# Optimization experiments

Measured on AMD Instinct MI355X. Metric: run time of the kernel, lower is better.

## Reference

```python
import jax, jax.numpy as jnp
import numpy as np

D_MODEL = 2048
N_HEAD = 16
HEAD_DIM = D_MODEL // N_HEAD
SCALE = 1.0 / (HEAD_DIM ** 0.5)


def setup_inputs() -> dict:
    key = jax.random.key(0)
    kx, kq, kk, kv, ko = jax.random.split(key, 5)
    std = 1.0 / np.sqrt(D_MODEL)
    return {
        "x": jax.random.normal(kx, (2, 2048, D_MODEL), dtype=jnp.float32),
        "w_q": jax.random.normal(kq, (D_MODEL, D_MODEL), dtype=jnp.float32) * std,
        "w_k": jax.random.normal(kk, (D_MODEL, D_MODEL), dtype=jnp.float32) * std,
        "w_v": jax.random.normal(kv, (D_MODEL, D_MODEL), dtype=jnp.float32) * std,
        "w_o": jax.random.normal(ko, (D_MODEL, D_MODEL), dtype=jnp.float32) * std,
    }


def reference(x, w_q, w_k, w_v, w_o):
    b, s, d = x.shape
    # nn.Linear(d,d,bias=False): y = x @ W^T, weights stored [out, in]
    def proj(w):
        y = jnp.einsum("bsd,ed->bse", x, w)
        return y.reshape(b, s, N_HEAD, HEAD_DIM).transpose(0, 2, 1, 3)  # [b,h,s,hd]
    q, k, v = proj(w_q), proj(w_k), proj(w_v)
    scores = jnp.einsum("bhqd,bhkd->bhqk", q, k) * SCALE  # [b,h,s,s]
    probs = jax.nn.softmax(scores, axis=-1)
    attn = jnp.einsum("bhqk,bhkd->bhqd", probs, v)
    attn = attn.transpose(0, 2, 1, 3).reshape(b, s, d)
    return jnp.einsum("bsd,ed->bse", attn, w_o)
```

## Files before the change

### kernel.cpp

```cpp
#include <hip/hip_runtime.h>

#define D_MODEL 2048
#define SEQ 2048
#define BATCH 2
#define NH 16
#define HD 128
#define MTOT 4096
#define NQKV 6144
#define QSTRIDE 4096

static constexpr float SCALE_LOG2E = 0.08838834764831845f * 1.4426950408889634f;

typedef __bf16 bf16x8 __attribute__((ext_vector_type(8)));
typedef _Float16 f16x4 __attribute__((ext_vector_type(4)));
typedef float f32x4 __attribute__((ext_vector_type(4)));

__device__ inline unsigned short f2bf(float f) {
  unsigned int u = __builtin_bit_cast(unsigned int, f);
  u += 0x7fffu + ((u >> 16) & 1u);
  return (unsigned short)(u >> 16);
}

__device__ inline float fast_exp2(float x) {
#if __has_builtin(__builtin_amdgcn_exp2f)
  return __builtin_amdgcn_exp2f(x);
#else
  return exp2f(x);
#endif
}

__device__ inline void gload_lds16(const void* g, void* s) {
  __builtin_amdgcn_global_load_lds(
      (__attribute__((address_space(1))) void*)g,
      (__attribute__((address_space(3))) void*)s, 16, 0, 0);
}

__global__ __launch_bounds__(256) void cvt_all(
    const float* __restrict__ x, const float* __restrict__ wq,
    const float* __restrict__ wk, const float* __restrict__ wv,
    const float* __restrict__ wo, unsigned short* __restrict__ xb,
    unsigned short* __restrict__ wqkv, unsigned short* __restrict__ wob) {
  const int y = blockIdx.y;
  const float* src;
  unsigned short* dst;
  int n4;
  if (y == 0) { src = x; dst = xb; n4 = MTOT * D_MODEL / 4; }
  else if (y == 4) { src = wo; dst = wob; n4 = D_MODEL * D_MODEL / 4; }
  else {
    src = (y == 1) ? wq : (y == 2) ? wk : wv;
    dst = wqkv + (size_t)(y - 1) * D_MODEL * D_MODEL;
    n4 = D_MODEL * D_MODEL / 4;
  }
  int i = blockIdx.x * 256 + threadIdx.x;
  if (i < n4) {
    float4 v = ((const float4*)src)[i];
    ushort4 o;
    o.x = f2bf(v.x); o.y = f2bf(v.y); o.z = f2bf(v.z); o.w = f2bf(v.w);
    ((ushort4*)dst)[i] = o;
  }
}

__global__ __launch_bounds__(256, 2) void gemm_qkv(
    const unsigned short* __restrict__ A, const unsigned short* __restrict__ B,
    unsigned short* __restrict__ QK, unsigned short* __restrict__ Vt) {
  __shared__ __align__(16) union {
    struct { unsigned short As[128 * 32]; unsigned short Bs[128 * 32]; } s;
    unsigned short T[128 * 136];
  } u;
  unsigned short* As = u.s.As;
  unsigned short* Bs = u.s.Bs;
  const int K = D_MODEL;
  const int tid = threadIdx.x;
  const int lane = tid & 63;
  const int wave = tid >> 6;
  const int quad = lane >> 4;
  const int l15 = lane & 15;
  const int m0 = blockIdx.y * 128;
  const int n0 = blockIdx.x * 128;
  const int wm = (wave >> 1) * 64;
  const int wn = (wave & 1) * 64;

  const int c0 = wave * 2, c1 = wave * 2 + 1;
  const int srow = lane >> 2;
  const int sr0 = c0 * 16 + srow;
  const int sr1 = c1 * 16 + srow;
  const int sk = (((lane & 3) ^ (srow & 3))) * 8;
  const unsigned short* Ag0 = A + (size_t)(m0 + sr0) * K + sk;
  const unsigned short* Ag1 = A + (size_t)(m0 + sr1) * K + sk;
  const unsigned short* Bg0 = B + (size_t)(n0 + sr0) * K + sk;
  const unsigned short* Bg1 = B + (size_t)(n0 + sr1) * K + sk;
  unsigned short* lA0 = As + c0 * 512;
  unsigned short* lA1 = As + c1 * 512;
  unsigned short* lB0 = Bs + c0 * 512;
  unsigned short* lB1 = Bs + c1 * 512;

  f32x4 acc[4][4] = {};
  const int axor = (quad ^ (l15 & 3)) * 8;

  for (int k0 = 0; k0 < K; k0 += 32) {
    __syncthreads();
    gload_lds16(Ag0 + k0, lA0);
    gload_lds16(Ag1 + k0, lA1);
    gload_lds16(Bg0 + k0, lB0);
    gload_lds16(Bg1 + k0, lB1);
    __builtin_amdgcn_s_waitcnt(0);
    __syncthreads();
    bf16x8 a[4], b[4];
#pragma unroll
    for (int i = 0; i < 4; i++)
      a[i] = *(const bf16x8*)(As + (wm + i * 16 + l15) * 32 + axor);
#pragma unroll
    for (int j = 0; j < 4; j++)
      b[j] = *(const bf16x8*)(Bs + (wn + j * 16 + l15) * 32 + axor);
#pragma unroll
    for (int i = 0; i < 4; i++)
#pragma unroll
      for (int j = 0; j < 4; j++)
        acc[i][j] = __builtin_amdgcn_mfma_f32_16x16x32_bf16(a[i], b[j], acc[i][j], 0, 0, 0);
  }

  const int er = quad * 4;
  const int ec = l15;
  if (n0 < 4096) {
#pragma unroll
    for (int i = 0; i < 4; i++)
#pragma unroll
      for (int j = 0; j < 4; j++) {
        const int mm = m0 + wm + i * 16 + er;
        const int nn = n0 + wn + j * 16 + ec;
#pragma unroll
        for (int r = 0; r < 4; r++)
          QK[(size_t)(mm + r) * QSTRIDE + nn] = f2bf(acc[i][j][r]);
      }
  } else {
    __syncthreads();
    const int vcol0 = n0 - 4096;
    const int h = vcol0 >> 7;
    const int b = m0 >> 11;
    const int bh = b * NH + h;
    const int sbase = m0 & (SEQ - 1);
#pragma unroll
    for (int i = 0; i < 4; i++)
#pragma unroll
      for (int j = 0; j < 4; j++) {
        const int dl = wn + j * 16 + ec;
        const int sl = wm + i * 16 + er;
        f16x4 hv;
#pragma unroll
        for (int r = 0; r < 4; r++) hv[r] = (_Float16)acc[i][j][r];
        *(f16x4*)(u.T + dl * 136 + sl) = hv;
      }
    __syncthreads();
#pragma unroll
    for (int p = 0; p < 8; p++) {
      const int d = p * 16 + (tid >> 4);
      const int s = (tid & 15) * 8;
      float4 chunk = *(const float4*)(u.T + d * 136 + s);
      *(float4*)(Vt + ((size_t)(bh * HD + d)) * SEQ + sbase + s) = chunk;
    }
  }
}

__global__ __launch_bounds__(256, 4) void gemm_out(
    const unsigned short* __restrict__ A, const unsigned short* __restrict__ B,
    float* __restrict__ C, int M, int N, int K) {
  __shared__ __align__(16) unsigned short As[128 * 32];
  __shared__ __align__(16) unsigned short Bs[64 * 32];
  const int tid = threadIdx.x;
  const int lane = tid & 63;
  const int wave = tid >> 6;
  const int quad = lane >> 4;
  const int l15 = lane & 15;
  const int m0 = blockIdx.y * 128;
  const int n0 = blockIdx.x * 64;
  const int wm = (wave >> 1) * 64;
  const int wn = (wave & 1) * 32;

  const int srow = lane >> 2;
  const int sk = (((lane & 3) ^ (srow & 3))) * 8;
  const unsigned short* Ag0 = A + (size_t)(m0 + wave * 32 + srow) * K + sk;
  const unsigned short* Ag1 = A + (size_t)(m0 + wave * 32 + 16 + srow) * K + sk;
  unsigned short* lA0 = As + (wave * 2) * 512;
  unsigned short* lA1 = As + (wave * 2 + 1) * 512;
  const unsigned short* Bg = B + (size_t)(n0 + wave * 16 + srow) * K + sk;
  unsigned short* lB = Bs + wave * 512;

  f32x4 acc[4][2] = {};
  const int axor = (quad ^ (l15 & 3)) * 8;

  for (int k0 = 0; k0 < K; k0 += 32) {
    __syncthreads();
    gload_lds16(Ag0 + k0, lA0);
    gload_lds16(Ag1 + k0, lA1);
    gload_lds16(Bg + k0, lB);
    __builtin_amdgcn_s_waitcnt(0);
    __syncthreads();
    bf16x8 a[4], b[2];
#pragma unroll
    for (int i = 0; i < 4; i++)
      a[i] = *(const bf16x8*)(As + (wm + i * 16 + l15) * 32 + axor);
#pragma unroll
    for (int j = 0; j < 2; j++)
      b[j] = *(const bf16x8*)(Bs + (wn + j * 16 + l15) * 32 + axor);
#pragma unroll
    for (int i = 0; i < 4; i++)
#pragma unroll
      for (int j = 0; j < 2; j++)
        acc[i][j] = __builtin_amdgcn_mfma_f32_16x16x32_bf16(a[i], b[j], acc[i][j], 0, 0, 0);
  }

  const int er = quad * 4;
  const int ec = l15;
#pragma unroll
  for (int i = 0; i < 4; i++)
#pragma unroll
    for (int j = 0; j < 2; j++) {
      const int mm = m0 + wm + i * 16 + er;
      const int nn = n0 + wn + j * 16 + ec;
#pragma unroll
      for (int r = 0; r < 4; r++)
        C[(size_t)(mm + r) * N + nn] = acc[i][j][r];
    }
}

__global__ __launch_bounds__(256, 2) void flash_attn(
    const unsigned short* __restrict__ QK, const unsigned short* __restrict__ Vt,
    unsigned short* __restrict__ Og) {
  __shared__ __align__(16) unsigned short Ks[2][64 * 128];
  __shared__ __align__(16) unsigned short Vs[2][128 * 64];
  const int tid = threadIdx.x;
  const int lane = tid & 63;
  const int wave = tid >> 6;
  const int quad = lane >> 4;
  const int l15 = lane & 15;
  const int id = blockIdx.x;
  const int xr = id & 7;
  const int kk = id >> 3;
  const int bh = xr * 4 + (kk >> 4);
  const int b = bh >> 4, h = bh & 15;
  const int q0 = (kk & 15) * 128;

  const size_t kbase = (size_t)(b * SEQ) * QSTRIDE + D_MODEL + h * HD;
  const size_t vbase = (size_t)bh * HD * SEQ;

  bf16x8 qf[2][4];
#pragma unroll
  for (int t = 0; t < 2; t++)
#pragma unroll
    for (int kc = 0; kc < 4; kc++)
      qf[t][kc] = *(const bf16x8*)(QK + (size_t)(b * SEQ + q0 + wave * 32 + t * 16 + l15) * QSTRIDE +
                                   h * HD + kc * 32 + quad * 8);

  const unsigned short* kg[4];
  const unsigned short* vg[4];
  int klofs[4], vlofs[4];
#pragma unroll
  for (int i = 0; i < 4; i++) {
    int krow = wave * 16 + i * 4 + quad;
    int kc_ = l15 ^ (i * 4 + quad);
    kg[i] = QK + kbase + (size_t)krow * QSTRIDE + kc_ * 8;
    klofs[i] = (wave * 16 + i * 4) * 128;
    int vrow = wave * 32 + i * 8 + (lane >> 3);
    int vc_ = (lane & 7) ^ (lane >> 3);
    vg[i] = Vt + vbase + (size_t)vrow * SEQ + vc_ * 8;
    vlofs[i] = (wave * 32 + i * 8) * 64;
  }

#pragma unroll
  for (int i = 0; i < 4; i++) gload_lds16(kg[i], &Ks[0][klofs[i]]);
#pragma unroll
  for (int i = 0; i < 4; i++) gload_lds16(vg[i], &Vs[0][vlofs[i]]);
#pragma unroll
  for (int i = 0; i < 4; i++) { kg[i] += 64 * QSTRIDE; vg[i] += 64; }
  __builtin_amdgcn_s_waitcnt(0);
  __syncthreads();

  float lsum[2] = {0.f, 0.f};
  f32x4 Oa[2][8] = {};

  for (int it = 0; it < SEQ / 64; ++it) {
    const int cur = it & 1;
    if (it < SEQ / 64 - 1) {
#pragma unroll
      for (int i = 0; i < 4; i++) gload_lds16(kg[i], &Ks[cur ^ 1][klofs[i]]);
#pragma unroll
      for (int i = 0; i < 4; i++) gload_lds16(vg[i], &Vs[cur ^ 1][vlofs[i]]);
#pragma unroll
      for (int i = 0; i < 4; i++) { kg[i] += 64 * QSTRIDE; vg[i] += 64; }
    }

    const unsigned short* kb = &Ks[cur][0];
    f32x4 sacc[2][4] = {};
#pragma unroll
    for (int js = 0; js < 4; js++)
#pragma unroll
      for (int kc = 0; kc < 4; kc++) {
        bf16x8 kf = *(const bf16x8*)(kb + (js * 16 + l15) * 128 + (((kc * 4 + quad) ^ l15) * 8));
        sacc[0][js] = __builtin_amdgcn_mfma_f32_16x16x32_bf16(kf, qf[0][kc], sacc[0][js], 0, 0, 0);
        sacc[1][js] = __builtin_amdgcn_mfma_f32_16x16x32_bf16(kf, qf[1][kc], sacc[1][js], 0, 0, 0);
      }

    f16x4 pb[2][4];
#pragma unroll
    for (int t = 0; t < 2; t++)
#pragma unroll
      for (int js = 0; js < 4; js++)
#pragma unroll
        for (int r = 0; r < 4; r++) {
          float p = fast_exp2(sacc[t][js][r] * SCALE_LOG2E);
          lsum[t] += p;
          pb[t][js][r] = (_Float16)p;
        }

    const unsigned short* vb_ = &Vs[cur][0];
#pragma unroll
    for (int jt = 0; jt < 8; jt++)
#pragma unroll
      for (int js = 0; js < 4; js++) {
        f16x4 vf = *(const f16x4*)(vb_ + (jt * 16 + l15) * 64 +
                                   (((js * 2 + (quad >> 1)) ^ (lane & 7)) * 8) + (quad & 1) * 4);
        Oa[0][jt] = __builtin_amdgcn_mfma_f32_16x16x16f16(vf, pb[0][js], Oa[0][jt], 0, 0, 0);
        Oa[1][jt] = __builtin_amdgcn_mfma_f32_16x16x16f16(vf, pb[1][js], Oa[1][jt], 0, 0, 0);
      }

    __builtin_amdgcn_s_waitcnt(0);
    __syncthreads();
  }

  float inv[2];
#pragma unroll
  for (int t = 0; t < 2; t++) {
    float s = lsum[t];
    s += __shfl_xor(s, 16);
    s += __shfl_xor(s, 32);
    inv[t] = 1.0f / s;
  }

#pragma unroll
  for (int t = 0; t < 2; t++) {
    const size_t rowbase = (size_t)(b * SEQ + q0 + wave * 32 + t * 16 + l15) * D_MODEL + h * HD;
#pragma unroll
    for (int jt = 0; jt < 8; jt++) {
      ushort4 o;
      o.x = f2bf(Oa[t][jt][0] * inv[t]);
      o.y = f2bf(Oa[t][jt][1] * inv[t]);
      o.z = f2bf(Oa[t][jt][2] * inv[t]);
      o.w = f2bf(Oa[t][jt][3] * inv[t]);
      *(ushort4*)(Og + rowbase + jt * 16 + quad * 4) = o;
    }
  }
}

extern "C" void kernel_launch(void* const* d_in, const int* in_sizes, int n_in,
                              void* d_out, int out_size, void* d_ws, size_t ws_size,
                              hipStream_t stream) {
  const float* x = (const float*)d_in[0];
  const float* wq = (const float*)d_in[1];
  const float* wk = (const float*)d_in[2];
  const float* wv = (const float*)d_in[3];
  const float* wo = (const float*)d_in[4];
  float* out = (float*)d_out;
  char* ws = (char*)d_ws;
  const size_t MB = 1u << 20;
  if (ws_size < 96 * MB) return;

  unsigned short* xb = (unsigned short*)(ws);
  unsigned short* wqkv = (unsigned short*)(ws + 16 * MB);
  unsigned short* wob = (unsigned short*)(ws + 40 * MB);
  unsigned short* QKb = (unsigned short*)(ws + 48 * MB);
  unsigned short* Vtb = (unsigned short*)(ws + 80 * MB);
  unsigned short* Ab = xb;

  cvt_all<<<dim3(8192, 5), 256, 0, stream>>>(x, wq, wk, wv, wo, xb, wqkv, wob);

  gemm_qkv<<<dim3(NQKV / 128, MTOT / 128), 256, 0, stream>>>(xb, wqkv, QKb, Vtb);

  flash_attn<<<512, 256, 0, stream>>>(QKb, Vtb, Ab);

  gemm_out<<<dim3(D_MODEL / 64, MTOT / 128), 256, 0, stream>>>(Ab, wob, out, MTOT, D_MODEL, D_MODEL);
}
```

Measured before the change: 392.4 us.

## Split Q/K buffers, widen attention blocks to 8 waves, split-K output GEMM

The fused QK buffer becomes separate contiguous Q and K buffers, so K rows load with stride D_MODEL instead of 4096. Flash attention now runs 512 threads per block, with each wave owning 16 query rows instead of 32. This halves per-wave registers and shares each K/V tile across more waves, though it doubles the LDS reads per MFMA. The output GEMM moves to 128x128 tiles with two wave groups, each handling half of K, and the partial sums are reduced through LDS. That raises arithmetic intensity but adds a serialized reduction epilogue and fewer blocks.

```diff
diff --git a/kernel.cpp b/kernel.cpp
--- a/kernel.cpp
+++ b/kernel.cpp
@@ -7,7 +7,6 @@
 #define HD 128
 #define MTOT 4096
 #define NQKV 6144
-#define QSTRIDE 4096
 
 static constexpr float SCALE_LOG2E = 0.08838834764831845f * 1.4426950408889634f;
 
@@ -62,7 +61,8 @@
 
 __global__ __launch_bounds__(256, 2) void gemm_qkv(
     const unsigned short* __restrict__ A, const unsigned short* __restrict__ B,
-    unsigned short* __restrict__ QK, unsigned short* __restrict__ Vt) {
+    unsigned short* __restrict__ Qb, unsigned short* __restrict__ Kb,
+    unsigned short* __restrict__ Vt) {
   __shared__ __align__(16) union {
     struct { unsigned short As[128 * 32]; unsigned short Bs[128 * 32]; } s;
     unsigned short T[128 * 136];
@@ -82,13 +82,11 @@
 
   const int c0 = wave * 2, c1 = wave * 2 + 1;
   const int srow = lane >> 2;
-  const int sr0 = c0 * 16 + srow;
-  const int sr1 = c1 * 16 + srow;
   const int sk = (((lane & 3) ^ (srow & 3))) * 8;
-  const unsigned short* Ag0 = A + (size_t)(m0 + sr0) * K + sk;
-  const unsigned short* Ag1 = A + (size_t)(m0 + sr1) * K + sk;
-  const unsigned short* Bg0 = B + (size_t)(n0 + sr0) * K + sk;
-  const unsigned short* Bg1 = B + (size_t)(n0 + sr1) * K + sk;
+  const unsigned short* Ag0 = A + (size_t)(m0 + c0 * 16 + srow) * K + sk;
+  const unsigned short* Ag1 = A + (size_t)(m0 + c1 * 16 + srow) * K + sk;
+  const unsigned short* Bg0 = B + (size_t)(n0 + c0 * 16 + srow) * K + sk;
+  const unsigned short* Bg1 = B + (size_t)(n0 + c1 * 16 + srow) * K + sk;
   unsigned short* lA0 = As + c0 * 512;
   unsigned short* lA1 = As + c1 * 512;
   unsigned short* lB0 = Bs + c0 * 512;
@@ -122,15 +120,17 @@
   const int er = quad * 4;
   const int ec = l15;
   if (n0 < 4096) {
+    unsigned short* Dst = (n0 < 2048) ? Qb : Kb;
+    const int nb = (n0 < 2048) ? n0 : (n0 - 2048);
 #pragma unroll
     for (int i = 0; i < 4; i++)
 #pragma unroll
       for (int j = 0; j < 4; j++) {
         const int mm = m0 + wm + i * 16 + er;
-        const int nn = n0 + wn + j * 16 + ec;
+        const int nn = nb + wn + j * 16 + ec;
 #pragma unroll
         for (int r = 0; r < 4; r++)
-          QK[(size_t)(mm + r) * QSTRIDE + nn] = f2bf(acc[i][j][r]);
+          Dst[(size_t)(mm + r) * D_MODEL + nn] = f2bf(acc[i][j][r]);
       }
   } else {
     __syncthreads();
@@ -161,71 +161,89 @@
   }
 }
 
-__global__ __launch_bounds__(256, 4) void gemm_out(
+__global__ __launch_bounds__(512, 4) void gemm_out(
     const unsigned short* __restrict__ A, const unsigned short* __restrict__ B,
     float* __restrict__ C, int M, int N, int K) {
-  __shared__ __align__(16) unsigned short As[128 * 32];
-  __shared__ __align__(16) unsigned short Bs[64 * 32];
+  __shared__ __align__(16) unsigned short As[2][128 * 32];
+  __shared__ __align__(16) unsigned short Bs[2][128 * 32];
   const int tid = threadIdx.x;
   const int lane = tid & 63;
   const int wave = tid >> 6;
+  const int g = wave >> 2;
+  const int w = wave & 3;
   const int quad = lane >> 4;
   const int l15 = lane & 15;
   const int m0 = blockIdx.y * 128;
-  const int n0 = blockIdx.x * 64;
-  const int wm = (wave >> 1) * 64;
-  const int wn = (wave & 1) * 32;
-
+  const int n0 = blockIdx.x * 128;
+  const int wm = (w >> 1) * 64;
+  const int wn = (w & 1) * 64;
+  const int kb = g * (D_MODEL / 2);
+
+  const int c0 = w * 2, c1 = w * 2 + 1;
   const int srow = lane >> 2;
   const int sk = (((lane & 3) ^ (srow & 3))) * 8;
-  const unsigned short* Ag0 = A + (size_t)(m0 + wave * 32 + srow) * K + sk;
-  const unsigned short* Ag1 = A + (size_t)(m0 + wave * 32 + 16 + srow) * K + sk;
-  unsigned short* lA0 = As + (wave * 2) * 512;
-  unsigned short* lA1 = As + (wave * 2 + 1) * 512;
-  const unsigned short* Bg = B + (size_t)(n0 + wave * 16 + srow) * K + sk;
-  unsigned short* lB = Bs + wave * 512;
-
-  f32x4 acc[4][2] = {};
+  const unsigned short* Ag0 = A + (size_t)(m0 + c0 * 16 + srow) * K + kb + sk;
+  const unsigned short* Ag1 = A + (size_t)(m0 + c1 * 16 + srow) * K + kb + sk;
+  const unsigned short* Bg0 = B + (size_t)(n0 + c0 * 16 + srow) * K + kb + sk;
+  const unsigned short* Bg1 = B + (size_t)(n0 + c1 * 16 + srow) * K + kb + sk;
+  unsigned short* lA0 = As[g] + c0 * 512;
+  unsigned short* lA1 = As[g] + c1 * 512;
+  unsigned short* lB0 = Bs[g] + c0 * 512;
+  unsigned short* lB1 = Bs[g] + c1 * 512;
+
+  f32x4 acc[4][4] = {};
   const int axor = (quad ^ (l15 & 3)) * 8;
 
-  for (int k0 = 0; k0 < K; k0 += 32) {
+  for (int k0 = 0; k0 < D_MODEL / 2; k0 += 32) {
     __syncthreads();
     gload_lds16(Ag0 + k0, lA0);
     gload_lds16(Ag1 + k0, lA1);
-    gload_lds16(Bg + k0, lB);
+    gload_lds16(Bg0 + k0, lB0);
+    gload_lds16(Bg1 + k0, lB1);
     __builtin_amdgcn_s_waitcnt(0);
     __syncthreads();
-    bf16x8 a[4], b[2];
-#pragma unroll
-    for (int i = 0; i < 4; i++)
-      a[i] = *(const bf16x8*)(As + (wm + i * 16 + l15) * 32 + axor);
-#pragma unroll
-    for (int j = 0; j < 2; j++)
-      b[j] = *(const bf16x8*)(Bs + (wn + j * 16 + l15) * 32 + axor);
-#pragma unroll
-    for (int i = 0; i < 4; i++)
-#pragma unroll
-      for (int j = 0; j < 2; j++)
+    bf16x8 a[4], b[4];
+#pragma unroll
+    for (int i = 0; i < 4; i++)
+      a[i] = *(const bf16x8*)(As[g] + (wm + i * 16 + l15) * 32 + axor);
+#pragma unroll
+    for (int j = 0; j < 4; j++)
+      b[j] = *(const bf16x8*)(Bs[g] + (wn + j * 16 + l15) * 32 + axor);
+#pragma unroll
+    for (int i = 0; i < 4; i++)
+#pragma unroll
+      for (int j = 0; j < 4; j++)
         acc[i][j] = __builtin_amdgcn_mfma_f32_16x16x32_bf16(a[i], b[j], acc[i][j], 0, 0, 0);
   }
 
-  const int er = quad * 4;
-  const int ec = l15;
-#pragma unroll
-  for (int i = 0; i < 4; i++)
-#pragma unroll
-    for (int j = 0; j < 2; j++) {
-      const int mm = m0 + wm + i * 16 + er;
-      const int nn = n0 + wn + j * 16 + ec;
-#pragma unroll
-      for (int r = 0; r < 4; r++)
-        C[(size_t)(mm + r) * N + nn] = acc[i][j][r];
+  float* R = (float*)&As[0][0];
+  const int ridx = w * 1104 + lane * 17;
+#pragma unroll 1
+  for (int i = 0; i < 4; i++) {
+    __syncthreads();
+    if (g == 1) {
+#pragma unroll
+      for (int j = 0; j < 4; j++)
+#pragma unroll
+        for (int r = 0; r < 4; r++) R[ridx + j * 4 + r] = acc[i][j][r];
     }
-}
-
-__global__ __launch_bounds__(256, 2) void flash_attn(
-    const unsigned short* __restrict__ QK, const unsigned short* __restrict__ Vt,
-    unsigned short* __restrict__ Og) {
+    __syncthreads();
+    if (g == 0) {
+      const int mm = m0 + wm + i * 16 + quad * 4;
+#pragma unroll
+      for (int j = 0; j < 4; j++) {
+        const int nn = n0 + wn + j * 16 + l15;
+#pragma unroll
+        for (int r = 0; r < 4; r++)
+          C[(size_t)(mm + r) * N + nn] = acc[i][j][r] + R[ridx + j * 4 + r];
+      }
+    }
+  }
+}
+
+__global__ __launch_bounds__(512, 4) void flash_attn(
+    const unsigned short* __restrict__ Q, const unsigned short* __restrict__ Kg,
+    const unsigned short* __restrict__ Vt, unsigned short* __restrict__ Og) {
   __shared__ __align__(16) unsigned short Ks[2][64 * 128];
   __shared__ __align__(16) unsigned short Vs[2][128 * 64];
   const int tid = threadIdx.x;
@@ -234,83 +252,77 @@
   const int quad = lane >> 4;
   const int l15 = lane & 15;
   const int id = blockIdx.x;
-  const int xr = id & 7;
-  const int kk = id >> 3;
-  const int bh = xr * 4 + (kk >> 4);
+  const int bh = id >> 4;
   const int b = bh >> 4, h = bh & 15;
-  const int q0 = (kk & 15) * 128;
-
-  const size_t kbase = (size_t)(b * SEQ) * QSTRIDE + D_MODEL + h * HD;
+  const int q0 = (id & 15) * 128;
+
+  const size_t kbase = (size_t)(b * SEQ) * D_MODEL + h * HD;
   const size_t vbase = (size_t)bh * HD * SEQ;
 
-  bf16x8 qf[2][4];
-#pragma unroll
-  for (int t = 0; t < 2; t++)
-#pragma unroll
-    for (int kc = 0; kc < 4; kc++)
-      qf[t][kc] = *(const bf16x8*)(QK + (size_t)(b * SEQ + q0 + wave * 32 + t * 16 + l15) * QSTRIDE +
-                                   h * HD + kc * 32 + quad * 8);
-
-  const unsigned short* kg[4];
-  const unsigned short* vg[4];
-  int klofs[4], vlofs[4];
-#pragma unroll
-  for (int i = 0; i < 4; i++) {
-    int krow = wave * 16 + i * 4 + quad;
-    int kc_ = l15 ^ (i * 4 + quad);
-    kg[i] = QK + kbase + (size_t)krow * QSTRIDE + kc_ * 8;
-    klofs[i] = (wave * 16 + i * 4) * 128;
-    int vrow = wave * 32 + i * 8 + (lane >> 3);
-    int vc_ = (lane & 7) ^ (lane >> 3);
+  bf16x8 qf[4];
+#pragma unroll
+  for (int kc = 0; kc < 4; kc++)
+    qf[kc] = *(const bf16x8*)(Q + (size_t)(b * SEQ + q0 + wave * 16 + l15) * D_MODEL +
+                              h * HD + kc * 32 + quad * 8);
+
+  const unsigned short* kg[2];
+  const unsigned short* vg[2];
+  int klofs[2], vlofs[2];
+#pragma unroll
+  for (int i = 0; i < 2; i++) {
+    const int ck = wave * 2 + i;
+    const int krow = ck * 4 + quad;
+    const int kc_ = l15 ^ (krow & 15);
+    kg[i] = Kg + kbase + (size_t)krow * D_MODEL + kc_ * 8;
+    klofs[i] = ck * 512;
+    const int vrow = ck * 8 + (lane >> 3);
+    const int vc_ = (lane & 7) ^ (lane >> 3);
     vg[i] = Vt + vbase + (size_t)vrow * SEQ + vc_ * 8;
-    vlofs[i] = (wave * 32 + i * 8) * 64;
-  }
-
-#pragma unroll
-  for (int i = 0; i < 4; i++) gload_lds16(kg[i], &Ks[0][klofs[i]]);
-#pragma unroll
-  for (int i = 0; i < 4; i++) gload_lds16(vg[i], &Vs[0][vlofs[i]]);
-#pragma unroll
-  for (int i = 0; i < 4; i++) { kg[i] += 64 * QSTRIDE; vg[i] += 64; }
+    vlofs[i] = ck * 512;
+  }
+
+#pragma unroll
+  for (int i = 0; i < 2; i++) gload_lds16(kg[i], &Ks[0][klofs[i]]);
+#pragma unroll
+  for (int i = 0; i < 2; i++) gload_lds16(vg[i], &Vs[0][vlofs[i]]);
+#pragma unroll
+  for (int i = 0; i < 2; i++) { kg[i] += 64 * D_MODEL; vg[i] += 64; }
   __builtin_amdgcn_s_waitcnt(0);
   __syncthreads();
 
-  float lsum[2] = {0.f, 0.f};
-  f32x4 Oa[2][8] = {};
+  float lsum = 0.f;
+  f32x4 Oa[8] = {};
 
   for (int it = 0; it < SEQ / 64; ++it) {
     const int cur = it & 1;
     if (it < SEQ / 64 - 1) {
 #pragma unroll
-      for (int i = 0; i < 4; i++) gload_lds16(kg[i], &Ks[cur ^ 1][klofs[i]]);
-#pragma unroll
-      for (int i = 0; i < 4; i++) gload_lds16(vg[i], &Vs[cur ^ 1][vlofs[i]]);
-#pragma unroll
-      for (int i = 0; i < 4; i++) { kg[i] += 64 * QSTRIDE; vg[i] += 64; }
+      for (int i = 0; i < 2; i++) gload_lds16(kg[i], &Ks[cur ^ 1][klofs[i]]);
+#pragma unroll
+      for (int i = 0; i < 2; i++) gload_lds16(vg[i], &Vs[cur ^ 1][vlofs[i]]);
+#pragma unroll
+      for (int i = 0; i < 2; i++) { kg[i] += 64 * D_MODEL; vg[i] += 64; }
     }
 
     const unsigned short* kb = &Ks[cur][0];
-    f32x4 sacc[2][4] = {};
+    f32x4 sacc[4] = {};
 #pragma unroll
     for (int js = 0; js < 4; js++)
 #pragma unroll
       for (int kc = 0; kc < 4; kc++) {
         bf16x8 kf = *(const bf16x8*)(kb + (js * 16 + l15) * 128 + (((kc * 4 + quad) ^ l15) * 8));
-        sacc[0][js] = __builtin_amdgcn_mfma_f32_16x16x32_bf16(kf, qf[0][kc], sacc[0][js], 0, 0, 0);
-        sacc[1][js] = __builtin_amdgcn_mfma_f32_16x16x32_bf16(kf, qf[1][kc], sacc[1][js], 0, 0, 0);
-      }
-
-    f16x4 pb[2][4];
-#pragma unroll
-    for (int t = 0; t < 2; t++)
-#pragma unroll
-      for (int js = 0; js < 4; js++)
-#pragma unroll
-        for (int r = 0; r < 4; r++) {
-          float p = fast_exp2(sacc[t][js][r] * SCALE_LOG2E);
-          lsum[t] += p;
-          pb[t][js][r] = (_Float16)p;
-        }
+        sacc[js] = __builtin_amdgcn_mfma_f32_16x16x32_bf16(kf, qf[kc], sacc[js], 0, 0, 0);
+      }
+
+    f16x4 pb[4];
+#pragma unroll
+    for (int js = 0; js < 4; js++)
+#pragma unroll
+      for (int r = 0; r < 4; r++) {
+        float p = fast_exp2(sacc[js][r] * SCALE_LOG2E);
+        lsum += p;
+        pb[js][r] = (_Float16)p;
+      }
 
     const unsigned short* vb_ = &Vs[cur][0];
 #pragma unroll
@@ -319,35 +331,27 @@
       for (int js = 0; js < 4; js++) {
         f16x4 vf = *(const f16x4*)(vb_ + (jt * 16 + l15) * 64 +
                                    (((js * 2 + (quad >> 1)) ^ (lane & 7)) * 8) + (quad & 1) * 4);
-        Oa[0][jt] = __builtin_amdgcn_mfma_f32_16x16x16f16(vf, pb[0][js], Oa[0][jt], 0, 0, 0);
-        Oa[1][jt] = __builtin_amdgcn_mfma_f32_16x16x16f16(vf, pb[1][js], Oa[1][jt], 0, 0, 0);
+        Oa[jt] = __builtin_amdgcn_mfma_f32_16x16x16f16(vf, pb[js], Oa[jt], 0, 0, 0);
       }
 
     __builtin_amdgcn_s_waitcnt(0);
     __syncthreads();
   }
 
-  float inv[2];
-#pragma unroll
-  for (int t = 0; t < 2; t++) {
-    float s = lsum[t];
-    s += __shfl_xor(s, 16);
-    s += __shfl_xor(s, 32);
-    inv[t] = 1.0f / s;
-  }
-
-#pragma unroll
-  for (int t = 0; t < 2; t++) {
-    const size_t rowbase = (size_t)(b * SEQ + q0 + wave * 32 + t * 16 + l15) * D_MODEL + h * HD;
-#pragma unroll
-    for (int jt = 0; jt < 8; jt++) {
-      ushort4 o;
-      o.x = f2bf(Oa[t][jt][0] * inv[t]);
-      o.y = f2bf(Oa[t][jt][1] * inv[t]);
-      o.z = f2bf(Oa[t][jt][2] * inv[t]);
-      o.w = f2bf(Oa[t][jt][3] * inv[t]);
-      *(ushort4*)(Og + rowbase + jt * 16 + quad * 4) = o;
-    }
+  float s = lsum;
+  s += __shfl_xor(s, 16);
+  s += __shfl_xor(s, 32);
+  const float inv = 1.0f / s;
+
+  const size_t rowbase = (size_t)(b * SEQ + q0 + wave * 16 + l15) * D_MODEL + h * HD;
+#pragma unroll
+  for (int jt = 0; jt < 8; jt++) {
+    ushort4 o;
+    o.x = f2bf(Oa[jt][0] * inv);
+    o.y = f2bf(Oa[jt][1] * inv);
+    o.z = f2bf(Oa[jt][2] * inv);
+    o.w = f2bf(Oa[jt][3] * inv);
+    *(ushort4*)(Og + rowbase + jt * 16 + quad * 4) = o;
   }
 }
 
@@ -367,15 +371,16 @@
   unsigned short* xb = (unsigned short*)(ws);
   unsigned short* wqkv = (unsigned short*)(ws + 16 * MB);
   unsigned short* wob = (unsigned short*)(ws + 40 * MB);
-  unsigned short* QKb = (unsigned short*)(ws + 48 * MB);
+  unsigned short* Qb = (unsigned short*)(ws + 48 * MB);
+  unsigned short* Kb = (unsigned short*)(ws + 64 * MB);
   unsigned short* Vtb = (unsigned short*)(ws + 80 * MB);
   unsigned short* Ab = xb;
 
   cvt_all<<<dim3(8192, 5), 256, 0, stream>>>(x, wq, wk, wv, wo, xb, wqkv, wob);
 
-  gemm_qkv<<<dim3(NQKV / 128, MTOT / 128), 256, 0, stream>>>(xb, wqkv, QKb, Vtb);
-
-  flash_attn<<<512, 256, 0, stream>>>(QKb, Vtb, Ab);
-
-  gemm_out<<<dim3(D_MODEL / 64, MTOT / 128), 256, 0, stream>>>(Ab, wob, out, MTOT, D_MODEL, D_MODEL);
-}
+  gemm_qkv<<<dim3(NQKV / 128, MTOT / 128), 256, 0, stream>>>(xb, wqkv, Qb, Kb, Vtb);
+
+  flash_attn<<<512, 512, 0, stream>>>(Qb, Kb, Vtb, Ab);
+
+  gemm_out<<<dim3(D_MODEL / 128, MTOT / 128), 512, 0, stream>>>(Ab, wob, out, MTOT, D_MODEL, D_MODEL);
+}
```

After: 1.061 ms. +170.4%, slower.
